# Kernel tuning notes

Hardware: AMD Instinct MI355X
Metric: run time of the kernel (lower is better)

## Reference

```python
import jax, jax.numpy as jnp
import numpy as np

B, S, DEG, D, L = 16, 512, 8, 512, 64
E = B * S * DEG  # edges per direction
EPS = 1e-5


def _layernorm(x, g, b):
    mu = jnp.mean(x, axis=-1, keepdims=True)
    var = jnp.mean((x - mu) ** 2, axis=-1, keepdims=True)
    return (x - mu) * jax.lax.rsqrt(var + EPS) * g + b


def setup_inputs() -> dict:
    key = jax.random.key(0)
    ks = jax.random.split(key, 16)
    src = jax.random.normal(ks[0], (B, S, D), jnp.float32)
    arc_tensor_in = jnp.stack([
        jax.random.randint(ks[1], (E,), 0, B),
        jax.random.randint(ks[2], (E,), 0, S)]).astype(jnp.int32)
    label_tensor_in = jax.random.randint(ks[3], (E,), 0, L).astype(jnp.int32)
    arc_tensor_out = jnp.stack([
        jax.random.randint(ks[4], (E,), 0, B),
        jax.random.randint(ks[5], (E,), 0, S)]).astype(jnp.int32)
    label_tensor_out = jax.random.randint(ks[6], (E,), 0, L).astype(jnp.int32)
    mask_in = (jax.random.uniform(ks[7], (B * S, DEG)) > 0.2).astype(jnp.float32)
    mask_out = (jax.random.uniform(ks[8], (B * S, DEG)) > 0.2).astype(jnp.float32)
    mask_loop = jnp.ones((B * S, 1), jnp.float32)
    sent_mask = jnp.ones((B, S), jnp.float32)
    sc = np.float32(1.0 / np.sqrt(D))  # ~xavier scale
    V_in = jax.random.normal(ks[9], (D, D), jnp.float32) * sc
    V_out = jax.random.normal(ks[10], (D, D), jnp.float32) * sc
    W_self_loop = jax.random.normal(ks[11], (D, D), jnp.float32) * sc
    V_in_gate = jax.random.normal(ks[12], (D, 1), jnp.float32) * sc
    V_out_gate = jax.random.normal(ks[13], (D, 1), jnp.float32) * sc
    W_self_loop_gate = jax.random.normal(ks[14], (D, 1), jnp.float32) * sc
    b_in = jnp.zeros((L, D), jnp.float32)
    b_out = jnp.zeros((L, D), jnp.float32)
    b_in_gate = jnp.ones((L, 1), jnp.float32)
    b_out_gate = jnp.ones((L, 1), jnp.float32)
    ln_gamma = jnp.ones((D,), jnp.float32)
    ln_beta = jnp.zeros((D,), jnp.float32)
    return dict(src=src, arc_tensor_in=arc_tensor_in, label_tensor_in=label_tensor_in,
                arc_tensor_out=arc_tensor_out, label_tensor_out=label_tensor_out,
                mask_in=mask_in, mask_out=mask_out, mask_loop=mask_loop, sent_mask=sent_mask,
                V_in=V_in, b_in=b_in, V_in_gate=V_in_gate, b_in_gate=b_in_gate,
                V_out=V_out, b_out=b_out, V_out_gate=V_out_gate, b_out_gate=b_out_gate,
                W_self_loop=W_self_loop, W_self_loop_gate=W_self_loop_gate,
                ln_gamma=ln_gamma, ln_beta=ln_beta)


def reference(src, arc_tensor_in, label_tensor_in, arc_tensor_out, label_tensor_out,
              mask_in, mask_out, mask_loop, sent_mask,
              V_in, b_in, V_in_gate, b_in_gate, V_out, b_out, V_out_gate, b_out_gate,
              W_self_loop, W_self_loop_gate, ln_gamma, ln_beta):
    x = src.reshape(B * S, D)  # batch_first=True, dropout p=0 -> identity
    idx_in = arc_tensor_in[0] * S + arc_tensor_in[1]    # (E,)
    idx_out = arc_tensor_out[0] * S + arc_tensor_out[1]

    # in-arcs: gather projected node features + label bias
    in_ = (x @ V_in)[idx_in] + b_in[label_tensor_in]                    # (E, D)
    in_g = (x @ V_in_gate)[idx_in] + b_in_gate[label_tensor_in]         # (E, 1)
    # out-arcs
    out_ = (x @ V_out)[idx_out] + b_out[label_tensor_out]
    out_g = (x @ V_out_gate)[idx_out] + b_out_gate[label_tensor_out]
    # self loop
    loop_ = x @ W_self_loop                                             # (B*S, D)
    loop_g = x @ W_self_loop_gate                                       # (B*S, 1)

    pot = jnp.concatenate([in_.reshape(B * S, DEG, D),
                           out_.reshape(B * S, DEG, D),
                           loop_[:, None, :]], axis=1)                  # (B*S, 2*DEG+1, D)
    gate = jnp.concatenate([in_g.reshape(B * S, DEG),
                            out_g.reshape(B * S, DEG),
                            loop_g], axis=1)                            # (B*S, 2*DEG+1)
    mask_soft = jnp.concatenate([mask_in, mask_out, mask_loop], axis=1)

    probs = jax.nn.sigmoid(gate) * mask_soft
    h = jnp.sum(pot * probs[:, :, None], axis=1)                        # (B*S, D)

    sm = sent_mask.reshape(B * S, 1)
    h = _layernorm(h, ln_gamma, ln_beta) * sm
    h = jax.nn.relu(h)
    out = h.reshape(B, S, D) * sent_mask[:, :, None]
    return out + src  # residual
```

## Files before the change

kernel.cpp:

```cpp
#include <hip/hip_runtime.h>
#include <cstdint>
#include <cstddef>

#define DDIM   512
#define NNODES 8192
#define NEDGE  65536
#define PCOLS  1536
#define NKT    16
#define TILE_SHORTS 4096

typedef __attribute__((ext_vector_type(8))) short bf16x8;
typedef __attribute__((ext_vector_type(4))) float f32x4;

#define AS1 __attribute__((address_space(1)))
#define AS3 __attribute__((address_space(3)))

static __device__ __forceinline__ unsigned short f2bf(float f) {
    unsigned u = __float_as_uint(f);
    u += 0x7FFFu + ((u >> 16) & 1u);
    return (unsigned short)(u >> 16);
}

static __device__ __forceinline__ void unpack8(uint4 pv, float* pf) {
    const unsigned* pw = (const unsigned*)&pv;
    pf[0] = __uint_as_float(pw[0] << 16); pf[1] = __uint_as_float(pw[0] & 0xffff0000u);
    pf[2] = __uint_as_float(pw[1] << 16); pf[3] = __uint_as_float(pw[1] & 0xffff0000u);
    pf[4] = __uint_as_float(pw[2] << 16); pf[5] = __uint_as_float(pw[2] & 0xffff0000u);
    pf[6] = __uint_as_float(pw[3] << 16); pf[7] = __uint_as_float(pw[3] & 0xffff0000u);
}

__global__ __launch_bounds__(512) void prep_kernel(
    const float* __restrict__ src,
    const float* __restrict__ vg_in, const float* __restrict__ vg_out,
    const float* __restrict__ vg_loop,
    const float* __restrict__ v_in, const float* __restrict__ v_out,
    const float* __restrict__ w_loop, const float* __restrict__ b_in,
    const float* __restrict__ b_out,
    unsigned short* __restrict__ xbt, unsigned short* __restrict__ wct,
    unsigned short* __restrict__ bb_in, unsigned short* __restrict__ bb_out,
    float* __restrict__ g_in, float* __restrict__ g_out, float* __restrict__ g_loop)
{
    __shared__ float tile[64][65];
    if (blockIdx.x < 1024) {
        int lane = threadIdx.x & 63;
        int row  = blockIdx.x * 8 + (threadIdx.x >> 6);
        int j0   = lane * 8;

        const float* x = src + (size_t)row * DDIM + j0;
        float4 x0 = *(const float4*)x;
        float4 x1 = *(const float4*)(x + 4);
        float xs[8] = {x0.x, x0.y, x0.z, x0.w, x1.x, x1.y, x1.z, x1.w};

        alignas(16) unsigned short h[8];
#pragma unroll
        for (int i = 0; i < 8; ++i) h[i] = f2bf(xs[i]);
        int tm = row >> 7, rw = row & 127;
        size_t off = ((size_t)(tm * NKT + (lane >> 2))) * TILE_SHORTS
                   + ((size_t)(lane & 3) * 128 + rw) * 8;
        *(uint4*)(xbt + off) = *(const uint4*)h;

        float s0 = 0.f, s1 = 0.f, s2 = 0.f;
#pragma unroll
        for (int i = 0; i < 8; ++i) {
            s0 += xs[i] * vg_in[j0 + i];
            s1 += xs[i] * vg_out[j0 + i];
            s2 += xs[i] * vg_loop[j0 + i];
        }
#pragma unroll
        for (int o = 32; o > 0; o >>= 1) {
            s0 += __shfl_xor(s0, o);
            s1 += __shfl_xor(s1, o);
            s2 += __shfl_xor(s2, o);
        }
        if (lane == 0) { g_in[row] = s0; g_out[row] = s1; g_loop[row] = s2; }
    } else if (blockIdx.x < 1216) {
        int bb = blockIdx.x - 1024;
        int kc = bb / 24;
        int nt = bb % 24;
        int k0 = kc * 64;

        const float* srcp; int nl0 = (nt & 7) * 64;
        if      (nt < 8)  srcp = v_in;
        else if (nt < 16) srcp = v_out;
        else              srcp = w_loop;

        int c  = threadIdx.x & 63;
        int rr = threadIdx.x >> 6;
#pragma unroll
        for (int i = 0; i < 8; ++i) {
            int kk = i * 8 + rr;
            tile[kk][c] = srcp[(size_t)(k0 + kk) * DDIM + nl0 + c];
        }
        __syncthreads();
        int tn = nt >> 1;
        int nrbase = (nt & 1) * 64;
        int idx = threadIdx.x;
        int nn  = idx >> 3;
        int k8  = idx & 7;
        int ktl = k8 >> 2;
        int kb  = k8 & 3;
        size_t tb = ((size_t)(tn * NKT + kc * 2 + ktl)) * TILE_SHORTS;
        alignas(16) unsigned short h[8];
#pragma unroll
        for (int e = 0; e < 8; ++e) h[e] = f2bf(tile[k8 * 8 + e][nn]);
        *(uint4*)(wct + tb + ((size_t)kb * 128 + nrbase + nn) * 8) = *(const uint4*)h;
    } else {
        int i = (blockIdx.x - 1216) * 512 + threadIdx.x;
        int base = i * 4;
        int which = base >> 15;
        int off   = base & 32767;
        const float* s = which ? b_out : b_in;
        unsigned short* d = which ? bb_out : bb_in;
        float4 v = *(const float4*)(s + off);
        alignas(8) unsigned short h[4] = {f2bf(v.x), f2bf(v.y), f2bf(v.z), f2bf(v.w)};
        *(uint2*)(d + off) = *(const uint2*)h;
    }
}

__global__ __launch_bounds__(512, 6) void gemmp_kernel(
    const unsigned short* __restrict__ At,
    const unsigned short* __restrict__ Bt,
    unsigned short* __restrict__ P)
{
    __shared__ short lds_a[3][TILE_SHORTS];
    __shared__ short lds_b[3][TILE_SHORTS];

    int tid  = threadIdx.x;
    int lane = tid & 63;
    int wid  = tid >> 6;
    int bid  = blockIdx.x;
    int local = bid >> 3;
    int tm    = (bid & 7) * 8 + local / 12;
    int tn    = local % 12;
    int row0 = tm * 128, col0 = tn * 128;
    int wm   = wid >> 2, wn = wid & 3;
    int r16  = lane & 15, kq = lane >> 4;

    f32x4 acc[4][2];
#pragma unroll
    for (int m = 0; m < 4; ++m)
#pragma unroll
        for (int n = 0; n < 2; ++n) acc[m][n] = (f32x4){0.f, 0.f, 0.f, 0.f};

    const unsigned short* ga = At + (size_t)(tm * NKT) * TILE_SHORTS;
    const unsigned short* gb = Bt + (size_t)(tn * NKT) * TILE_SHORTS;

    auto stage = [&](int buf, int kt) {
        size_t kt8 = (size_t)kt * TILE_SHORTS;
        __builtin_amdgcn_global_load_lds(
            (const AS1 void*)(ga + kt8 + tid * 8),
            (AS3 void*)(&lds_a[buf][wid * 512]), 16, 0, 0);
        __builtin_amdgcn_global_load_lds(
            (const AS1 void*)(gb + kt8 + tid * 8),
            (AS3 void*)(&lds_b[buf][wid * 512]), 16, 0, 0);
    };

    auto compute = [&](int buf) {
        const short* la = lds_a[buf];
        const short* lb = lds_b[buf];
        bf16x8 af[4], bfr[2];
#pragma unroll
        for (int m = 0; m < 4; ++m)
            af[m] = *(const bf16x8*)(la + (kq * 128 + wm * 64 + m * 16 + r16) * 8);
#pragma unroll
        for (int n = 0; n < 2; ++n)
            bfr[n] = *(const bf16x8*)(lb + (kq * 128 + wn * 32 + n * 16 + r16) * 8);
#pragma unroll
        for (int m = 0; m < 4; ++m)
#pragma unroll
            for (int n = 0; n < 2; ++n)
                acc[m][n] = __builtin_amdgcn_mfma_f32_16x16x32_bf16(
                    af[m], bfr[n], acc[m][n], 0, 0, 0);
        __builtin_amdgcn_sched_barrier(0);
        __builtin_amdgcn_s_barrier();
    };

    stage(0, 0); stage(1, 1);

    int bufc = 0;
    for (int t = 0; t < 14; ++t) {
        int bufs = bufc + 2; if (bufs >= 3) bufs -= 3;
        stage(bufs, t + 2);
        asm volatile("s_waitcnt vmcnt(4)" ::: "memory");
        __builtin_amdgcn_sched_barrier(0);
        __builtin_amdgcn_s_barrier();
        __builtin_amdgcn_sched_barrier(0);
        compute(bufc);
        ++bufc; if (bufc == 3) bufc = 0;
    }
    asm volatile("s_waitcnt vmcnt(2)" ::: "memory");
    __builtin_amdgcn_sched_barrier(0);
    __builtin_amdgcn_s_barrier();
    __builtin_amdgcn_sched_barrier(0);
    compute(bufc);
    ++bufc; if (bufc == 3) bufc = 0;
    asm volatile("s_waitcnt vmcnt(0)" ::: "memory");
    __builtin_amdgcn_sched_barrier(0);
    __builtin_amdgcn_s_barrier();
    __builtin_amdgcn_sched_barrier(0);
    compute(bufc);

#pragma unroll
    for (int m = 0; m < 4; ++m) {
        int grow = row0 + wm * 64 + m * 16 + kq * 4;
#pragma unroll
        for (int n = 0; n < 2; ++n) {
            int gcol = col0 + wn * 32 + n * 16 + r16;
#pragma unroll
            for (int r = 0; r < 4; ++r)
                P[(size_t)(grow + r) * PCOLS + gcol] = f2bf(acc[m][n][r]);
        }
    }
}

__global__ __launch_bounds__(512) void aggf_kernel(
    const unsigned short* __restrict__ P,
    const float* __restrict__ g_in, const float* __restrict__ g_out,
    const float* __restrict__ g_loop,
    const int* __restrict__ arc_in, const int* __restrict__ lbl_in,
    const int* __restrict__ arc_out, const int* __restrict__ lbl_out,
    const float* __restrict__ mask_in, const float* __restrict__ mask_out,
    const float* __restrict__ mask_loop, const float* __restrict__ sent_mask,
    const unsigned short* __restrict__ bb_in, const unsigned short* __restrict__ bb_out,
    const float* __restrict__ bg_in, const float* __restrict__ bg_out,
    const float* __restrict__ ln_g, const float* __restrict__ ln_b,
    const float* __restrict__ src, float* __restrict__ out)
{
    int lane = threadIdx.x & 63;
    int n    = blockIdx.x * 8 + (threadIdx.x >> 6);
    int j0   = lane * 8;

    float acc[8] = {0,0,0,0,0,0,0,0};

#pragma unroll
    for (int k = 0; k < 8; ++k) {
        int e  = n * 8 + k;
        float mk = mask_in[e];
        if (mk != 0.f) {
            int sn = arc_in[e] * 512 + arc_in[NEDGE + e];
            int lb = lbl_in[e];
            float w = mk / (1.0f + __expf(-(g_in[sn] + bg_in[lb])));
            uint4 pv = *(const uint4*)(P + (size_t)sn * PCOLS + j0);
            uint4 bv = *(const uint4*)(bb_in + (size_t)lb * DDIM + j0);
            float pf[8], bf[8]; unpack8(pv, pf); unpack8(bv, bf);
#pragma unroll
            for (int i = 0; i < 8; ++i) acc[i] += w * (pf[i] + bf[i]);
        }
    }
#pragma unroll
    for (int k = 0; k < 8; ++k) {
        int e  = n * 8 + k;
        float mk = mask_out[e];
        if (mk != 0.f) {
            int sn = arc_out[e] * 512 + arc_out[NEDGE + e];
            int lb = lbl_out[e];
            float w = mk / (1.0f + __expf(-(g_out[sn] + bg_out[lb])));
            uint4 pv = *(const uint4*)(P + (size_t)sn * PCOLS + 512 + j0);
            uint4 bv = *(const uint4*)(bb_out + (size_t)lb * DDIM + j0);
            float pf[8], bf[8]; unpack8(pv, pf); unpack8(bv, bf);
#pragma unroll
            for (int i = 0; i < 8; ++i) acc[i] += w * (pf[i] + bf[i]);
        }
    }
    {
        float wl = mask_loop[n] / (1.0f + __expf(-g_loop[n]));
        uint4 pv = *(const uint4*)(P + (size_t)n * PCOLS + 1024 + j0);
        float pf[8]; unpack8(pv, pf);
#pragma unroll
        for (int i = 0; i < 8; ++i) acc[i] += wl * pf[i];
    }

    float sum = 0.f, sq = 0.f;
#pragma unroll
    for (int i = 0; i < 8; ++i) { sum += acc[i]; sq += acc[i] * acc[i]; }
#pragma unroll
    for (int o = 32; o > 0; o >>= 1) {
        sum += __shfl_xor(sum, o);
        sq  += __shfl_xor(sq, o);
    }
    float mu   = sum * (1.0f / 512.0f);
    float var  = sq * (1.0f / 512.0f) - mu * mu;
    float rstd = rsqrtf(var + 1e-5f);
    float sm   = sent_mask[n];

    float4 gg0 = *(const float4*)(ln_g + j0);
    float4 gg1 = *(const float4*)(ln_g + j0 + 4);
    float4 be0 = *(const float4*)(ln_b + j0);
    float4 be1 = *(const float4*)(ln_b + j0 + 4);
    const float* sr = src + (size_t)n * DDIM + j0;
    float4 s0 = *(const float4*)sr;
    float4 s1 = *(const float4*)(sr + 4);
    float gl[8] = {gg0.x, gg0.y, gg0.z, gg0.w, gg1.x, gg1.y, gg1.z, gg1.w};
    float bt[8] = {be0.x, be0.y, be0.z, be0.w, be1.x, be1.y, be1.z, be1.w};
    float srs[8] = {s0.x, s0.y, s0.z, s0.w, s1.x, s1.y, s1.z, s1.w};

    float o_[8];
#pragma unroll
    for (int i = 0; i < 8; ++i) {
        float v = (acc[i] - mu) * rstd * gl[i] + bt[i];
        v *= sm;
        v = fmaxf(v, 0.f);
        o_[i] = v * sm + srs[i];
    }
    float4 w0 = {o_[0], o_[1], o_[2], o_[3]};
    float4 w1 = {o_[4], o_[5], o_[6], o_[7]};
    float* op = out + (size_t)n * DDIM + j0;
    *(float4*)op = w0;
    *(float4*)(op + 4) = w1;
}

extern "C" void kernel_launch(void* const* d_in, const int* in_sizes, int n_in,
                              void* d_out, int out_size, void* d_ws, size_t ws_size,
                              hipStream_t stream)
{
    const float* src       = (const float*)d_in[0];
    const int*   arc_in    = (const int*)d_in[1];
    const int*   lbl_in    = (const int*)d_in[2];
    const int*   arc_out   = (const int*)d_in[3];
    const int*   lbl_out   = (const int*)d_in[4];
    const float* mask_in   = (const float*)d_in[5];
    const float* mask_out  = (const float*)d_in[6];
    const float* mask_loop = (const float*)d_in[7];
    const float* sent_mask = (const float*)d_in[8];
    const float* V_in      = (const float*)d_in[9];
    const float* b_in      = (const float*)d_in[10];
    const float* Vg_in     = (const float*)d_in[11];
    const float* bg_in     = (const float*)d_in[12];
    const float* V_out     = (const float*)d_in[13];
    const float* b_out     = (const float*)d_in[14];
    const float* Vg_out    = (const float*)d_in[15];
    const float* bg_out    = (const float*)d_in[16];
    const float* W_loop    = (const float*)d_in[17];
    const float* Wg_loop   = (const float*)d_in[18];
    const float* ln_g      = (const float*)d_in[19];
    const float* ln_b      = (const float*)d_in[20];

    uint8_t* ws = (uint8_t*)d_ws;
    unsigned short* xbt   = (unsigned short*)(ws);
    unsigned short* wct   = (unsigned short*)(ws + 8388608);
    unsigned short* bb_in = (unsigned short*)(ws + 9961472);
    unsigned short* bb_out= (unsigned short*)(ws + 10027008);
    float*          g_in  = (float*)(ws + 10092544);
    float*          g_out = (float*)(ws + 10125312);
    float*          g_lp  = (float*)(ws + 10158080);
    unsigned short* P     = (unsigned short*)(ws + 10190848);

    prep_kernel<<<1248, 512, 0, stream>>>(src, Vg_in, Vg_out, Wg_loop,
                                          V_in, V_out, W_loop, b_in, b_out,
                                          xbt, wct, bb_in, bb_out,
                                          g_in, g_out, g_lp);
    gemmp_kernel<<<768, 512, 0, stream>>>(xbt, wct, P);
    aggf_kernel<<<1024, 512, 0, stream>>>(P, g_in, g_out, g_lp,
                                          arc_in, lbl_in, arc_out, lbl_out,
                                          mask_in, mask_out, mask_loop, sent_mask,
                                          bb_in, bb_out, bg_in, bg_out,
                                          ln_g, ln_b, src, (float*)d_out);
}
```

Baseline: 53.73 us.

## Split in/out edge aggregation across two waves per node with LDS reduction

The aggregation kernel now assigns two wavefronts per node: one handles in-arcs plus the self loop, the other handles out-arcs, and their partial sums are combined through shared memory before the layernorm epilogue. Edge indices and gate weights are loaded up front and the mask branch is removed, so all gathers can be issued back to back for more memory-level parallelism. The grid doubles to keep one node per wave pair. In exchange it adds a block barrier and LDS traffic, idles half the waves during the epilogue, and loads rows for masked-out edges that were previously skipped.

```diff
diff --git a/kernel.cpp b/kernel.cpp
--- a/kernel.cpp
+++ b/kernel.cpp
@@ -226,49 +226,75 @@
     const float* __restrict__ ln_g, const float* __restrict__ ln_b,
     const float* __restrict__ src, float* __restrict__ out)
 {
-    int lane = threadIdx.x & 63;
-    int n    = blockIdx.x * 8 + (threadIdx.x >> 6);
+    __shared__ float part[4][8][64];
+
+    int tid  = threadIdx.x;
+    int lane = tid & 63;
+    int wv   = tid >> 6;
+    int nl   = wv >> 1;
+    int role = wv & 1;
+    int n    = blockIdx.x * 4 + nl;
     int j0   = lane * 8;
 
     float acc[8] = {0,0,0,0,0,0,0,0};
 
-#pragma unroll
-    for (int k = 0; k < 8; ++k) {
-        int e  = n * 8 + k;
-        float mk = mask_in[e];
-        if (mk != 0.f) {
-            int sn = arc_in[e] * 512 + arc_in[NEDGE + e];
-            int lb = lbl_in[e];
-            float w = mk / (1.0f + __expf(-(g_in[sn] + bg_in[lb])));
-            uint4 pv = *(const uint4*)(P + (size_t)sn * PCOLS + j0);
-            uint4 bv = *(const uint4*)(bb_in + (size_t)lb * DDIM + j0);
+    if (role == 0) {
+        int sn[8], lb[8];
+        float w[8];
+#pragma unroll
+        for (int k = 0; k < 8; ++k) {
+            int e = n * 8 + k;
+            sn[k] = arc_in[e] * 512 + arc_in[NEDGE + e];
+            lb[k] = lbl_in[e];
+            w[k]  = mask_in[e];
+        }
+#pragma unroll
+        for (int k = 0; k < 8; ++k)
+            w[k] = w[k] / (1.0f + __expf(-(g_in[sn[k]] + bg_in[lb[k]])));
+#pragma unroll
+        for (int k = 0; k < 8; ++k) {
+            uint4 pv = *(const uint4*)(P + (size_t)sn[k] * PCOLS + j0);
+            uint4 bv = *(const uint4*)(bb_in + (size_t)lb[k] * DDIM + j0);
             float pf[8], bf[8]; unpack8(pv, pf); unpack8(bv, bf);
 #pragma unroll
-            for (int i = 0; i < 8; ++i) acc[i] += w * (pf[i] + bf[i]);
-        }
-    }
-#pragma unroll
-    for (int k = 0; k < 8; ++k) {
-        int e  = n * 8 + k;
-        float mk = mask_out[e];
-        if (mk != 0.f) {
-            int sn = arc_out[e] * 512 + arc_out[NEDGE + e];
-            int lb = lbl_out[e];
-            float w = mk / (1.0f + __expf(-(g_out[sn] + bg_out[lb])));
-            uint4 pv = *(const uint4*)(P + (size_t)sn * PCOLS + 512 + j0);
-            uint4 bv = *(const uint4*)(bb_out + (size_t)lb * DDIM + j0);
+            for (int i = 0; i < 8; ++i) acc[i] += w[k] * (pf[i] + bf[i]);
+        }
+        {
+            float wl = mask_loop[n] / (1.0f + __expf(-g_loop[n]));
+            uint4 pv = *(const uint4*)(P + (size_t)n * PCOLS + 1024 + j0);
+            float pf[8]; unpack8(pv, pf);
+#pragma unroll
+            for (int i = 0; i < 8; ++i) acc[i] += wl * pf[i];
+        }
+    } else {
+        int sn[8], lb[8];
+        float w[8];
+#pragma unroll
+        for (int k = 0; k < 8; ++k) {
+            int e = n * 8 + k;
+            sn[k] = arc_out[e] * 512 + arc_out[NEDGE + e];
+            lb[k] = lbl_out[e];
+            w[k]  = mask_out[e];
+        }
+#pragma unroll
+        for (int k = 0; k < 8; ++k)
+            w[k] = w[k] / (1.0f + __expf(-(g_out[sn[k]] + bg_out[lb[k]])));
+#pragma unroll
+        for (int k = 0; k < 8; ++k) {
+            uint4 pv = *(const uint4*)(P + (size_t)sn[k] * PCOLS + 512 + j0);
+            uint4 bv = *(const uint4*)(bb_out + (size_t)lb[k] * DDIM + j0);
             float pf[8], bf[8]; unpack8(pv, pf); unpack8(bv, bf);
 #pragma unroll
-            for (int i = 0; i < 8; ++i) acc[i] += w * (pf[i] + bf[i]);
-        }
-    }
-    {
-        float wl = mask_loop[n] / (1.0f + __expf(-g_loop[n]));
-        uint4 pv = *(const uint4*)(P + (size_t)n * PCOLS + 1024 + j0);
-        float pf[8]; unpack8(pv, pf);
-#pragma unroll
-        for (int i = 0; i < 8; ++i) acc[i] += wl * pf[i];
-    }
+            for (int i = 0; i < 8; ++i) acc[i] += w[k] * (pf[i] + bf[i]);
+        }
+#pragma unroll
+        for (int i = 0; i < 8; ++i) part[nl][i][lane] = acc[i];
+    }
+    __syncthreads();
+    if (role == 1) return;
+
+#pragma unroll
+    for (int i = 0; i < 8; ++i) acc[i] += part[nl][i][lane];
 
     float sum = 0.f, sq = 0.f;
 #pragma unroll
@@ -350,7 +376,7 @@
                                           xbt, wct, bb_in, bb_out,
                                           g_in, g_out, g_lp);
     gemmp_kernel<<<768, 512, 0, stream>>>(xbt, wct, P);
-    aggf_kernel<<<1024, 512, 0, stream>>>(P, g_in, g_out, g_lp,
+    aggf_kernel<<<2048, 512, 0, stream>>>(P, g_in, g_out, g_lp,
                                           arc_in, lbl_in, arc_out, lbl_out,
                                           mask_in, mask_out, mask_loop, sent_mask,
                                           bb_in, bb_out, bg_in, bg_out,
```

Measured after the change: 62.07 us. 1.16x slower.
